# Optimization experiments

Hardware: AMD Instinct MI355X
Metric: run time of the kernel (lower is better)

## Reference

```python
import jax, jax.numpy as jnp
import numpy as np

B, NIN, NH, SUB, HID = 8192, 1433, 64, 6, 128
TEMP, LAMB, ITERS = 0.4, 20.0, 5

def prelu(x, a):
    return jnp.where(x >= 0, x, a * x)

def l2norm(x):
    # F.normalize with eps clamp
    n = jnp.maximum(jnp.linalg.norm(x, axis=-1, keepdims=True), 1e-12)
    return x / n

def setup_inputs() -> dict:
    key = jax.random.key(0)
    ks = jax.random.split(key, 16)
    inp = {}
    inp['seq1'] = jax.random.normal(ks[0], (B, SUB, NIN), jnp.float32)
    inp['seq2'] = jax.random.normal(ks[1], (B, SUB, NIN), jnp.float32)
    inp['adj1'] = jax.random.uniform(ks[2], (B, SUB, SUB), jnp.float32)
    inp['adj2'] = jax.random.uniform(ks[3], (B, SUB, SUB), jnp.float32)
    inp['rescale_ratio'] = jax.random.uniform(ks[4], (B, SUB - 1, SUB - 1), jnp.float32)
    inp['gcn_W'] = jax.random.normal(ks[5], (NH, NIN), jnp.float32) / np.sqrt(NIN)
    inp['gcn_b'] = jnp.zeros((NH,), jnp.float32)
    inp['gcn_a'] = jnp.float32(0.25)
    inp['dec_W1'] = jax.random.normal(ks[6], (HID, NH * 4), jnp.float32) / np.sqrt(NH * 4)
    inp['dec_b1'] = jnp.zeros((HID,), jnp.float32)
    inp['dec_a1'] = jnp.float32(0.25)
    inp['dec_W2'] = jax.random.normal(ks[7], (HID, HID), jnp.float32) / np.sqrt(HID)
    inp['dec_b2'] = jnp.zeros((HID,), jnp.float32)
    inp['dec_a2'] = jnp.float32(0.25)
    inp['dec_W3'] = jax.random.normal(ks[8], (NIN, HID), jnp.float32) / np.sqrt(HID)
    inp['dec_b3'] = jnp.zeros((NIN,), jnp.float32)
    inp['dec_a3'] = jnp.float32(0.25)
    inp['disc_W'] = jax.random.normal(ks[9], (1, NH, NH), jnp.float32) / np.sqrt(NH)
    inp['disc_b'] = jnp.zeros((1,), jnp.float32)
    inp['subgraph_size'] = 4
    return inp

def sinkhorn_score(g1, n1, g2, n2, rescale_ratio):
    # cost has grad; transport is computed under no_grad in torch
    cost = (1.0 - jnp.einsum('bik,bjk->bij', l2norm(g1), l2norm(g2))) * rescale_ratio
    sg = jax.lax.stop_gradient
    g1s, n1s, g2s, n2s, costs = sg(g1), sg(n1), sg(g2), sg(n2), sg(cost)
    r = jnp.einsum('bik,bjk->bij', g1s, n2s)            # [B, N, 1]
    r = jnp.where(r <= 0, 1e-8, r)
    r = r / jnp.sum(r, axis=1, keepdims=True)
    c = jnp.einsum('bik,bjk->bij', g2s, n1s)            # [B, N, 1]
    c = jnp.where(c <= 0, 1e-8, c)
    c = c / jnp.sum(c, axis=1, keepdims=True)
    P = jnp.exp(-LAMB * costs)                          # [B, N, N]
    u = jnp.ones_like(c) / c.shape[1]
    for _ in range(ITERS):
        v = r / jnp.einsum('bij,bjk->bik', P, u)
        u = c / jnp.einsum('bji,bjk->bik', P, v)
    # diag(v) @ P @ diag(u)
    transport = v * P * jnp.swapaxes(u, 1, 2)           # [B, N, N]
    S = jnp.sum(transport * (1.0 - cost), axis=(1, 2))[:, None]  # [B, 1]
    return S

def reference(seq1, seq2, adj1, adj2, rescale_ratio, gcn_W, gcn_b, gcn_a,
              dec_W1, dec_b1, dec_a1, dec_W2, dec_b2, dec_a2, dec_W3, dec_b3, dec_a3,
              disc_W, disc_b, subgraph_size):
    def gcn(seq, adj):
        fts = jnp.einsum('bnf,hf->bnh', seq, gcn_W)
        return prelu(jnp.einsum('bnm,bmh->bnh', adj, fts) + gcn_b, gcn_a)
    h1 = gcn(seq1, adj1)   # [B, SUB, NH]
    h2 = gcn(seq2, adj2)
    # swap last two rows, then split graph-part / node-part
    def swap(h):
        return jnp.concatenate([h[:, :-2], h[:, -1:], h[:, -2:-1]], axis=1)
    h1n, h2n = swap(h1), swap(h2)
    g1, n1 = h1n[:, :-1], h1n[:, -1:]
    g2, n2 = h2n[:, :-1], h2n[:, -1:]
    S = sinkhorn_score(g1, n1, g2, n2, rescale_ratio)
    loss_pos = jnp.exp(S / TEMP) * 2.0                  # [B, 1]
    # decoder (subgraph_size=4 path): sub_node = h[:, :sub_size-2, :]
    x = h1[:, :subgraph_size, :].reshape(h1.shape[0], -1)
    x = prelu(x @ dec_W1.T + dec_b1, dec_a1)
    x = prelu(x @ dec_W2.T + dec_b2, dec_a2)
    node_recons = prelu(x @ dec_W3.T + dec_b3, dec_a3)  # [B, NIN]
    # discriminator (avg readout over context nodes, bilinear score)
    c = jnp.mean(h1[:, :-1, :], axis=1)                 # [B, NH]
    hp = h1[:, -1, :]                                   # [B, NH]
    s1 = jnp.einsum('bi,oij,bj->bo', hp, disc_W, c) + disc_b
    c_mi = jnp.concatenate([c[-2:-1], c[:-1]], axis=0)  # negsamp_round=1 shift
    s2 = jnp.einsum('bi,oij,bj->bo', hp, disc_W, c_mi) + disc_b
    logits = jnp.concatenate([s1, s2], axis=1)          # [B, 2]
    return jnp.concatenate([loss_pos, node_recons, logits], axis=1)  # [B, 1+NIN+2]
```

## Files before the change

### kernel.cpp

```cpp
#include <hip/hip_runtime.h>
#include <math.h>

#define BB   8192
#define NIN  1433
#define NH   64
#define SUBG 6
#define HID  128

typedef __attribute__((ext_vector_type(8))) short bf16x8;
typedef __attribute__((ext_vector_type(4))) float f32x4;
typedef __attribute__((ext_vector_type(16))) float f32x16;

__device__ __forceinline__ short f2bf(float x) {
  unsigned u = __float_as_uint(x);
  unsigned r = (u + 0x7fffu + ((u >> 16) & 1u)) >> 16;
  return (short)r;
}
__device__ __forceinline__ float bf2f(short s) {
  return __uint_as_float(((unsigned)(unsigned short)s) << 16);
}
__device__ __forceinline__ float allred64(float v) {
#pragma unroll
  for (int m = 1; m < 64; m <<= 1) v += __shfl_xor(v, m, 64);
  return v;
}

__device__ __forceinline__ void gload_lds16(const short* g, short* l) {
  __builtin_amdgcn_global_load_lds(
      (const __attribute__((address_space(1))) void*)g,
      (__attribute__((address_space(3))) void*)l, 16, 0, 0);
}

#define WAITV(N)                                            \
  {                                                         \
    asm volatile("s_waitcnt vmcnt(" #N ")" ::: "memory");   \
    __builtin_amdgcn_sched_barrier(0);                      \
  }
#define BARRIER()                                           \
  {                                                         \
    __builtin_amdgcn_s_barrier();                           \
    __builtin_amdgcn_sched_barrier(0);                      \
  }

__global__ void pack_kernel(const float* __restrict__ src, short* __restrict__ hi,
                            short* __restrict__ lo, int Oreal, int NF, int Kreal, int nchunk) {
  int idx = blockIdx.x * 256 + threadIdx.x;
  int total = nchunk * NF * 512;
  if (idx >= total) return;
  int j    = idx & 7;
  int lane = (idx >> 3) & 63;
  int nf   = (idx >> 9) % NF;
  int c    = idx / (NF * 512);
  int o = nf * 16 + (lane & 15);
  int k = c * 32 + ((lane >> 4) << 3) + j;
  float v = (o < Oreal && k < Kreal) ? src[(size_t)o * Kreal + k] : 0.f;
  short h = f2bf(v);
  hi[idx] = h;
  lo[idx] = f2bf(v - bf2f(h));
}

__global__ void pack32_kernel(const float* __restrict__ src, short* __restrict__ hi,
                              short* __restrict__ lo) {
  int idx = blockIdx.x * 256 + threadIdx.x;
  if (idx >= 45 * 4 * 512) return;
  int j    = idx & 7;
  int lane = (idx >> 3) & 63;
  int s    = (idx >> 9) & 3;
  int c    = idx >> 11;
  int o = (s & 1) * 32 + (lane & 31);
  int k = c * 32 + ((s >> 1) << 4) + ((lane >> 5) << 3) + j;
  float v = (k < NIN) ? src[(size_t)o * NIN + k] : 0.f;
  short h = f2bf(v);
  hi[idx] = h;
  lo[idx] = f2bf(v - bf2f(h));
}

__global__ __launch_bounds__(384, 3) void gcn_mfma(
    const float* __restrict__ seq1, const float* __restrict__ seq2,
    const short* __restrict__ Gh, const short* __restrict__ Gl,
    float* __restrict__ fts1, float* __restrict__ fts2)
{
  __shared__ short sB[4][4096];
  const int tid = threadIdx.x;
  const int sid = blockIdx.x >> 8;
  const int bb  = blockIdx.x & 255;
  const float* __restrict__ seq = sid ? seq2 : seq1;
  float* __restrict__ fout = sid ? fts2 : fts1;
  const int w = tid >> 6, lane = tid & 63;
  const int l31 = lane & 31, lg2 = lane >> 5;
  const int row0 = bb * 192 + w * 32;

  f32x16 acc[2];
#pragma unroll
  for (int i = 0; i < 16; ++i) { acc[0][i] = 0.f; acc[1][i] = 0.f; }

  const float* aptr = seq + (size_t)(row0 + l31) * NIN + lg2 * 8;

  auto STAGE = [&](int c, int slot) {
    short* sb = &sB[slot][0];
    const size_t cb = (size_t)c * 256;
#pragma unroll
    for (int i = 0; i < 2; ++i) {
      const int pb = (w * 128 + i * 64) & 511;
      const short* src = (pb < 256) ? (Gh + (cb + pb) * 8 + (size_t)lane * 8)
                                    : (Gl + (cb + (pb - 256)) * 8 + (size_t)lane * 8);
      gload_lds16(src, sb + (pb + lane) * 8);
    }
  };

#define ALOAD(c_, R_)                                                        \
  {                                                                          \
    const float* ad_ = aptr + (c_) * 32;                                     \
    asm volatile(                                                            \
        "global_load_dwordx4 %0, %4, off\n\t"                                \
        "global_load_dwordx4 %1, %4, off offset:16\n\t"                      \
        "global_load_dwordx4 %2, %4, off offset:64\n\t"                      \
        "global_load_dwordx4 %3, %4, off offset:80"                          \
        : "=&v"(R_[0]), "=&v"(R_[1]), "=&v"(R_[2]), "=&v"(R_[3])             \
        : "v"(ad_));                                                         \
  }

  auto SPLIT8 = [&](const f32x4& p, const f32x4& q, bf16x8& H, bf16x8& L) {
    float av[8] = {p[0], p[1], p[2], p[3], q[0], q[1], q[2], q[3]};
#pragma unroll
    for (int j = 0; j < 8; ++j) {
      unsigned u = __float_as_uint(av[j]);
      H[j] = (short)(u >> 16);
      L[j] = f2bf(av[j] - __uint_as_float(u & 0xffff0000u));
    }
  };

  auto COMPUTE = [&](int c, const f32x4* R) {
    bf16x8 Ah0, Al0, Ah1, Al1;
    SPLIT8(R[0], R[1], Ah0, Al0);
    SPLIT8(R[2], R[3], Ah1, Al1);
    const short* bs = &sB[c & 3][0];
    __builtin_amdgcn_s_setprio(1);
#pragma unroll
    for (int ct = 0; ct < 2; ++ct) {
      bf16x8 Bh0 = *(const bf16x8*)(bs + ((0 + ct) * 64 + lane) * 8);
      bf16x8 Bl0 = *(const bf16x8*)(bs + 2048 + ((0 + ct) * 64 + lane) * 8);
      bf16x8 Bh1 = *(const bf16x8*)(bs + ((2 + ct) * 64 + lane) * 8);
      bf16x8 Bl1 = *(const bf16x8*)(bs + 2048 + ((2 + ct) * 64 + lane) * 8);
      acc[ct] = __builtin_amdgcn_mfma_f32_32x32x16_bf16(Ah0, Bh0, acc[ct], 0, 0, 0);
      acc[ct] = __builtin_amdgcn_mfma_f32_32x32x16_bf16(Al0, Bh0, acc[ct], 0, 0, 0);
      acc[ct] = __builtin_amdgcn_mfma_f32_32x32x16_bf16(Ah0, Bl0, acc[ct], 0, 0, 0);
      acc[ct] = __builtin_amdgcn_mfma_f32_32x32x16_bf16(Ah1, Bh1, acc[ct], 0, 0, 0);
      acc[ct] = __builtin_amdgcn_mfma_f32_32x32x16_bf16(Al1, Bh1, acc[ct], 0, 0, 0);
      acc[ct] = __builtin_amdgcn_mfma_f32_32x32x16_bf16(Ah1, Bl1, acc[ct], 0, 0, 0);
    }
    __builtin_amdgcn_s_setprio(0);
  };

  f32x4 A0[4], A1[4];
  STAGE(0, 0); ALOAD(0, A0);
  STAGE(1, 1); ALOAD(1, A1);

#pragma unroll 1
  for (int cc = 0; cc < 42; cc += 2) {
    WAITV(6); BARRIER();
    COMPUTE(cc, A0);
    STAGE(cc + 2, (cc + 2) & 3); ALOAD(cc + 2, A0);
    WAITV(6); BARRIER();
    COMPUTE(cc + 1, A1);
    STAGE(cc + 3, (cc + 3) & 3); ALOAD(cc + 3, A1);
  }
  WAITV(6); BARRIER();
  COMPUTE(42, A0);
  WAITV(0); BARRIER();
  COMPUTE(43, A1);

  {
    const int k0 = 44 * 32 + lg2 * 8;
    float av[16];
#pragma unroll
    for (int j = 0; j < 8; ++j) {
      int ka = k0 + j, kb = k0 + 16 + j;
      av[j]     = (ka < NIN) ? aptr[44 * 32 + j] : 0.f;
      av[8 + j] = (kb < NIN) ? aptr[44 * 32 + 16 + j] : 0.f;
    }
    bf16x8 Ah0, Al0, Ah1, Al1;
#pragma unroll
    for (int j = 0; j < 8; ++j) {
      unsigned u = __float_as_uint(av[j]);
      Ah0[j] = (short)(u >> 16);
      Al0[j] = f2bf(av[j] - __uint_as_float(u & 0xffff0000u));
      u = __float_as_uint(av[8 + j]);
      Ah1[j] = (short)(u >> 16);
      Al1[j] = f2bf(av[8 + j] - __uint_as_float(u & 0xffff0000u));
    }
#pragma unroll
    for (int ct = 0; ct < 2; ++ct) {
      const size_t o0 = ((size_t)(44 * 4 + ct) * 64 + lane) * 8;
      const size_t o1 = ((size_t)(44 * 4 + 2 + ct) * 64 + lane) * 8;
      bf16x8 Bh0 = *(const bf16x8*)(Gh + o0);
      bf16x8 Bl0 = *(const bf16x8*)(Gl + o0);
      bf16x8 Bh1 = *(const bf16x8*)(Gh + o1);
      bf16x8 Bl1 = *(const bf16x8*)(Gl + o1);
      acc[ct] = __builtin_amdgcn_mfma_f32_32x32x16_bf16(Ah0, Bh0, acc[ct], 0, 0, 0);
      acc[ct] = __builtin_amdgcn_mfma_f32_32x32x16_bf16(Al0, Bh0, acc[ct], 0, 0, 0);
      acc[ct] = __builtin_amdgcn_mfma_f32_32x32x16_bf16(Ah0, Bl0, acc[ct], 0, 0, 0);
      acc[ct] = __builtin_amdgcn_mfma_f32_32x32x16_bf16(Ah1, Bh1, acc[ct], 0, 0, 0);
      acc[ct] = __builtin_amdgcn_mfma_f32_32x32x16_bf16(Al1, Bh1, acc[ct], 0, 0, 0);
      acc[ct] = __builtin_amdgcn_mfma_f32_32x32x16_bf16(Ah1, Bl1, acc[ct], 0, 0, 0);
    }
  }

#pragma unroll
  for (int ct = 0; ct < 2; ++ct)
#pragma unroll
    for (int reg = 0; reg < 16; ++reg) {
      int crow = (reg & 3) + 8 * (reg >> 2) + 4 * lg2;
      fout[(size_t)(row0 + crow) * 64 + ct * 32 + l31] = acc[ct][reg];
    }
#undef ALOAD
}

__global__ __launch_bounds__(256) void sink_kernel(
    const float* __restrict__ fts1, const float* __restrict__ fts2,
    const float* __restrict__ adj1, const float* __restrict__ adj2,
    const float* __restrict__ resc, const float* __restrict__ discW,
    const float* __restrict__ bias, const float* __restrict__ aP,
    float* __restrict__ out, float* __restrict__ tws, float* __restrict__ h1w)
{
  const int b = (blockIdx.x << 2) + (threadIdx.x >> 6);
  const int lane = threadIdx.x & 63;
  const float* F1 = fts1 + (size_t)b * 384;
  const float* F2 = fts2 + (size_t)b * 384;
  float f1[6], f2[6];
#pragma unroll
  for (int m = 0; m < 6; ++m) { f1[m] = F1[m * 64 + lane]; f2[m] = F2[m * 64 + lane]; }
  const float bv = bias[lane];
  const float a = aP[0];
  const float* A1 = adj1 + (size_t)b * 36;
  const float* A2 = adj2 + (size_t)b * 36;
  float h1v[6], h2v[6];
#pragma unroll
  for (int n = 0; n < 6; ++n) {
    float o1 = bv, o2 = bv;
#pragma unroll
    for (int m = 0; m < 6; ++m) {
      o1 = fmaf(A1[n * 6 + m], f1[m], o1);
      o2 = fmaf(A2[n * 6 + m], f2[m], o2);
    }
    h1v[n] = (o1 >= 0.f) ? o1 : a * o1;
    h2v[n] = (o2 >= 0.f) ? o2 : a * o2;
  }
#pragma unroll
  for (int n = 0; n < 6; ++n) h1w[(size_t)b * 384 + n * 64 + lane] = h1v[n];

  float g1[5], g2[5];
#pragma unroll
  for (int i = 0; i < 4; ++i) { g1[i] = h1v[i]; g2[i] = h2v[i]; }
  g1[4] = h1v[5]; g2[4] = h2v[5];
  const float n1 = h1v[4], n2 = h2v[4];

  {
    float cm = (g1[0] + g1[1] + g1[2] + g1[3] + n1) * 0.2f;
    float t = 0.f;
    const float4* W4 = (const float4*)discW;
#pragma unroll 4
    for (int jq = 0; jq < 16; ++jq) {
      float4 wv = W4[lane * 16 + jq];
      t = fmaf(wv.x, __shfl(cm, 4 * jq, 64), t);
      t = fmaf(wv.y, __shfl(cm, 4 * jq + 1, 64), t);
      t = fmaf(wv.z, __shfl(cm, 4 * jq + 2, 64), t);
      t = fmaf(wv.w, __shfl(cm, 4 * jq + 3, 64), t);
    }
    tws[(size_t)b * 64 + lane] = t;
  }

  float in1[5], in2[5];
#pragma unroll
  for (int i = 0; i < 5; ++i) {
    float s = allred64(g1[i] * g1[i]);
    in1[i] = 1.f / fmaxf(sqrtf(s), 1e-12f);
    s = allred64(g2[i] * g2[i]);
    in2[i] = 1.f / fmaxf(sqrtf(s), 1e-12f);
  }
  float cost[25], P[25];
#pragma unroll
  for (int i = 0; i < 5; ++i)
#pragma unroll
    for (int j = 0; j < 5; ++j) {
      float d = allred64(g1[i] * g2[j]);
      float cv = (1.f - d * in1[i] * in2[j]) * resc[(size_t)b * 25 + i * 5 + j];
      cost[i * 5 + j] = cv;
      P[i * 5 + j] = expf(-20.f * cv);
    }
  float r[5], c[5];
  float rs = 0.f, cs = 0.f;
#pragma unroll
  for (int i = 0; i < 5; ++i) {
    float d = allred64(g1[i] * n2); d = (d <= 0.f) ? 1e-8f : d; r[i] = d; rs += d;
    d = allred64(g2[i] * n1);       d = (d <= 0.f) ? 1e-8f : d; c[i] = d; cs += d;
  }
#pragma unroll
  for (int i = 0; i < 5; ++i) { r[i] = r[i] / rs; c[i] = c[i] / cs; }

  float u[5], v[5];
#pragma unroll
  for (int i = 0; i < 5; ++i) u[i] = 0.2f;
#pragma unroll
  for (int it = 0; it < 5; ++it) {
#pragma unroll
    for (int i = 0; i < 5; ++i) {
      float pv = 0.f;
#pragma unroll
      for (int j = 0; j < 5; ++j) pv = fmaf(P[i * 5 + j], u[j], pv);
      v[i] = r[i] / pv;
    }
#pragma unroll
    for (int i = 0; i < 5; ++i) {
      float pu = 0.f;
#pragma unroll
      for (int j = 0; j < 5; ++j) pu = fmaf(P[j * 5 + i], v[j], pu);
      u[i] = c[i] / pu;
    }
  }
  float S = 0.f;
#pragma unroll
  for (int i = 0; i < 5; ++i)
#pragma unroll
    for (int j = 0; j < 5; ++j)
      S += v[i] * P[i * 5 + j] * u[j] * (1.f - cost[i * 5 + j]);
  if (lane == 0) out[(size_t)b * 1436] = expf(S * 2.5f) * 2.f;
}

__global__ __launch_bounds__(64) void dec12_mfma(
    const float* __restrict__ h1,
    const short* __restrict__ B1h, const short* __restrict__ B1l,
    const float* __restrict__ b1, const float* __restrict__ a1P,
    const short* __restrict__ B2h, const short* __restrict__ B2l,
    const float* __restrict__ b2, const float* __restrict__ a2P,
    float* __restrict__ x3)
{
  __shared__ float xT[16][132];
  const int lane = threadIdx.x;
  const int l15 = lane & 15, lg = lane >> 4;
  const int r0 = blockIdx.x * 16;

  f32x4 acc[8];
#pragma unroll
  for (int i = 0; i < 8; ++i) acc[i] = (f32x4){0.f, 0.f, 0.f, 0.f};

#pragma unroll
  for (int c = 0; c < 8; ++c) {
    const float* ap = h1 + (size_t)(r0 + l15) * 384 + c * 32 + lg * 8;
    float4 p = *(const float4*)ap;
    float4 q = *(const float4*)(ap + 4);
    float av[8] = {p.x, p.y, p.z, p.w, q.x, q.y, q.z, q.w};
    bf16x8 Ah, Al;
#pragma unroll
    for (int j = 0; j < 8; ++j) { short h = f2bf(av[j]); Ah[j] = h; Al[j] = f2bf(av[j] - bf2f(h)); }
#pragma unroll
    for (int nf = 0; nf < 8; ++nf) {
      size_t off = (((size_t)(c * 8 + nf)) << 9) + (size_t)lane * 8;
      bf16x8 Bh = *(const bf16x8*)(B1h + off);
      bf16x8 Bl = *(const bf16x8*)(B1l + off);
      acc[nf] = __builtin_amdgcn_mfma_f32_16x16x32_bf16(Ah, Bh, acc[nf], 0, 0, 0);
      acc[nf] = __builtin_amdgcn_mfma_f32_16x16x32_bf16(Al, Bh, acc[nf], 0, 0, 0);
      acc[nf] = __builtin_amdgcn_mfma_f32_16x16x32_bf16(Ah, Bl, acc[nf], 0, 0, 0);
    }
  }
  {
    const float a1 = a1P[0];
#pragma unroll
    for (int nf = 0; nf < 8; ++nf) {
      int o = nf * 16 + l15;
      float bv = b1[o];
#pragma unroll
      for (int j = 0; j < 4; ++j) {
        float v = acc[nf][j] + bv;
        xT[lg * 4 + j][o] = (v >= 0.f) ? v : a1 * v;
      }
    }
  }
  __syncthreads();

#pragma unroll
  for (int i = 0; i < 8; ++i) acc[i] = (f32x4){0.f, 0.f, 0.f, 0.f};
#pragma unroll
  for (int c = 0; c < 4; ++c) {
    const float* ap = &xT[l15][c * 32 + lg * 8];
    float4 p = *(const float4*)ap;
    float4 q = *(const float4*)(ap + 4);
    float av[8] = {p.x, p.y, p.z, p.w, q.x, q.y, q.z, q.w};
    bf16x8 Ah, Al;
#pragma unroll
    for (int j = 0; j < 8; ++j) { short h = f2bf(av[j]); Ah[j] = h; Al[j] = f2bf(av[j] - bf2f(h)); }
#pragma unroll
    for (int nf = 0; nf < 8; ++nf) {
      size_t off = (((size_t)(c * 8 + nf)) << 9) + (size_t)lane * 8;
      bf16x8 Bh = *(const bf16x8*)(B2h + off);
      bf16x8 Bl = *(const bf16x8*)(B2l + off);
      acc[nf] = __builtin_amdgcn_mfma_f32_16x16x32_bf16(Ah, Bh, acc[nf], 0, 0, 0);
      acc[nf] = __builtin_amdgcn_mfma_f32_16x16x32_bf16(Al, Bh, acc[nf], 0, 0, 0);
      acc[nf] = __builtin_amdgcn_mfma_f32_16x16x32_bf16(Ah, Bl, acc[nf], 0, 0, 0);
    }
  }
  {
    const float a2 = a2P[0];
#pragma unroll
    for (int nf = 0; nf < 8; ++nf) {
      int o = nf * 16 + l15;
      float bv = b2[o];
#pragma unroll
      for (int j = 0; j < 4; ++j) {
        float v = acc[nf][j] + bv;
        v = (v >= 0.f) ? v : a2 * v;
        x3[(size_t)(r0 + lg * 4 + j) * 128 + o] = v;
      }
    }
  }
}

__global__ __launch_bounds__(64) void dec3_mfma(
    const float* __restrict__ x3,
    const short* __restrict__ B3h, const short* __restrict__ B3l,
    const float* __restrict__ b3, const float* __restrict__ a3P,
    float* __restrict__ out)
{
  const int lane = threadIdx.x;
  const int l15 = lane & 15, lg = lane >> 4;
  const int rowblk = blockIdx.x & 511;
  const int nfg = blockIdx.x >> 9;
  const int r0 = rowblk * 16;

  bf16x8 A3h[4], A3l[4];
#pragma unroll
  for (int c = 0; c < 4; ++c) {
    const float* ap = x3 + (size_t)(r0 + l15) * 128 + c * 32 + lg * 8;
    float4 p = *(const float4*)ap;
    float4 q = *(const float4*)(ap + 4);
    float av[8] = {p.x, p.y, p.z, p.w, q.x, q.y, q.z, q.w};
#pragma unroll
    for (int j = 0; j < 8; ++j) {
      short h = f2bf(av[j]); A3h[c][j] = h; A3l[c][j] = f2bf(av[j] - bf2f(h));
    }
  }
  const float a3 = a3P[0];
  for (int t = 0; t < 15; ++t) {
    const int nf = nfg * 15 + t;
    f32x4 acc = (f32x4){0.f, 0.f, 0.f, 0.f};
#pragma unroll
    for (int c = 0; c < 4; ++c) {
      size_t off = (((size_t)(c * 90 + nf)) << 9) + (size_t)lane * 8;
      bf16x8 Bh = *(const bf16x8*)(B3h + off);
      bf16x8 Bl = *(const bf16x8*)(B3l + off);
      acc = __builtin_amdgcn_mfma_f32_16x16x32_bf16(A3h[c], Bh, acc, 0, 0, 0);
      acc = __builtin_amdgcn_mfma_f32_16x16x32_bf16(A3l[c], Bh, acc, 0, 0, 0);
      acc = __builtin_amdgcn_mfma_f32_16x16x32_bf16(A3h[c], Bl, acc, 0, 0, 0);
    }
    const int o = nf * 16 + l15;
    if (o < NIN) {
      float bv = b3[o];
#pragma unroll
      for (int j = 0; j < 4; ++j) {
        float v = acc[j] + bv;
        v = (v >= 0.f) ? v : a3 * v;
        out[(size_t)(r0 + lg * 4 + j) * 1436 + 1 + o] = v;
      }
    }
  }
}

__global__ __launch_bounds__(256) void disc_kernel(
    const float* __restrict__ h1, const float* __restrict__ tws,
    const float* __restrict__ dbP, float* __restrict__ out)
{
  const int b = (blockIdx.x << 2) + (threadIdx.x >> 6);
  const int lane = threadIdx.x & 63;
  float hp = h1[((size_t)b * SUBG + 5) * NH + lane];
  float t0 = tws[(size_t)b * 64 + lane];
  int bp = (b == 0) ? (BB - 2) : (b - 1);
  float tp = tws[(size_t)bp * 64 + lane];
  float s1 = allred64(hp * t0);
  float s2 = allred64(hp * tp);
  if (lane == 0) {
    float db = dbP[0];
    out[(size_t)b * 1436 + 1434] = s1 + db;
    out[(size_t)b * 1436 + 1435] = s2 + db;
  }
}

extern "C" void kernel_launch(void* const* d_in, const int* in_sizes, int n_in,
                              void* d_out, int out_size, void* d_ws, size_t ws_size,
                              hipStream_t stream) {
  (void)in_sizes; (void)n_in; (void)out_size; (void)ws_size;
  const float* seq1  = (const float*)d_in[0];
  const float* seq2  = (const float*)d_in[1];
  const float* adj1  = (const float*)d_in[2];
  const float* adj2  = (const float*)d_in[3];
  const float* resc  = (const float*)d_in[4];
  const float* gcnW  = (const float*)d_in[5];
  const float* gcnB  = (const float*)d_in[6];
  const float* gcnA  = (const float*)d_in[7];
  const float* W1    = (const float*)d_in[8];
  const float* b1    = (const float*)d_in[9];
  const float* a1    = (const float*)d_in[10];
  const float* W2    = (const float*)d_in[11];
  const float* b2    = (const float*)d_in[12];
  const float* a2    = (const float*)d_in[13];
  const float* W3    = (const float*)d_in[14];
  const float* b3    = (const float*)d_in[15];
  const float* a3    = (const float*)d_in[16];
  const float* discW = (const float*)d_in[17];
  const float* discB = (const float*)d_in[18];

  float* fts1 = (float*)d_ws;
  float* fts2 = fts1 + (size_t)BB * SUBG * NH;
  float* h1   = fts2 + (size_t)BB * SUBG * NH;
  float* tws  = h1  + (size_t)BB * SUBG * NH;
  float* x3   = tws + (size_t)BB * 64;
  short* Gh   = (short*)(x3 + (size_t)BB * 128);
  short* Gl   = Gh  + 45 * 4 * 512;
  short* B1h  = Gl  + 45 * 4 * 512;
  short* B1l  = B1h + 8 * 8 * 512;
  short* B2h  = B1l + 8 * 8 * 512;
  short* B2l  = B2h + 4 * 8 * 512;
  short* B3h  = B2l + 4 * 8 * 512;
  short* B3l  = B3h + 4 * 90 * 512;
  float* out  = (float*)d_out;

  pack32_kernel<<<(45 * 4 * 512 + 255) / 256, 256, 0, stream>>>(gcnW, Gh, Gl);
  pack_kernel<<<(8 * 8 * 512 + 255) / 256, 256, 0, stream>>>(W1, B1h, B1l, 128, 8, 256, 8);
  pack_kernel<<<(4 * 8 * 512 + 255) / 256, 256, 0, stream>>>(W2, B2h, B2l, 128, 8, 128, 4);
  pack_kernel<<<(4 * 90 * 512 + 255) / 256, 256, 0, stream>>>(W3, B3h, B3l, 1433, 90, 128, 4);

  gcn_mfma<<<512, 384, 0, stream>>>(seq1, seq2, Gh, Gl, fts1, fts2);
  sink_kernel<<<2048, 256, 0, stream>>>(fts1, fts2, adj1, adj2, resc, discW, gcnB, gcnA,
                                        out, tws, h1);
  dec12_mfma<<<512, 64, 0, stream>>>(h1, B1h, B1l, b1, a1, B2h, B2l, b2, a2, x3);
  dec3_mfma<<<3072, 64, 0, stream>>>(x3, B3h, B3l, b3, a3, out);
  disc_kernel<<<2048, 256, 0, stream>>>(h1, tws, discB, out);
}
```

Baseline: 325.3 us.

## Load GCN weight fragments directly into registers instead of staging through LDS

The GCN projection kernel no longer stages packed bf16 hi/lo weight chunks into shared memory with global_load_lds and block barriers. Each wave now loads its B fragments straight from global (L2-resident) memory into registers, double-buffered alongside the A loads. With no barriers, the block shrinks to 4 waves with a 768-block grid. This removes LDS traffic and inter-wave synchronisation, but every wave now fetches the weights redundantly and needs more VGPRs.

```diff
diff --git a/kernel.cpp b/kernel.cpp
--- a/kernel.cpp
+++ b/kernel.cpp
@@ -25,20 +25,9 @@
   return v;
 }
 
-__device__ __forceinline__ void gload_lds16(const short* g, short* l) {
-  __builtin_amdgcn_global_load_lds(
-      (const __attribute__((address_space(1))) void*)g,
-      (__attribute__((address_space(3))) void*)l, 16, 0, 0);
-}
-
 #define WAITV(N)                                            \
   {                                                         \
     asm volatile("s_waitcnt vmcnt(" #N ")" ::: "memory");   \
-    __builtin_amdgcn_sched_barrier(0);                      \
-  }
-#define BARRIER()                                           \
-  {                                                         \
-    __builtin_amdgcn_s_barrier();                           \
     __builtin_amdgcn_sched_barrier(0);                      \
   }
 
@@ -75,38 +64,25 @@
   lo[idx] = f2bf(v - bf2f(h));
 }
 
-__global__ __launch_bounds__(384, 3) void gcn_mfma(
+__global__ __launch_bounds__(256, 3) void gcn_mfma(
     const float* __restrict__ seq1, const float* __restrict__ seq2,
     const short* __restrict__ Gh, const short* __restrict__ Gl,
     float* __restrict__ fts1, float* __restrict__ fts2)
 {
-  __shared__ short sB[4][4096];
   const int tid = threadIdx.x;
-  const int sid = blockIdx.x >> 8;
-  const int bb  = blockIdx.x & 255;
+  const int sid = (blockIdx.x >= 384);
+  const int bb  = sid ? (blockIdx.x - 384) : blockIdx.x;
   const float* __restrict__ seq = sid ? seq2 : seq1;
   float* __restrict__ fout = sid ? fts2 : fts1;
   const int w = tid >> 6, lane = tid & 63;
   const int l31 = lane & 31, lg2 = lane >> 5;
-  const int row0 = bb * 192 + w * 32;
+  const int row0 = bb * 128 + w * 32;
 
   f32x16 acc[2];
 #pragma unroll
   for (int i = 0; i < 16; ++i) { acc[0][i] = 0.f; acc[1][i] = 0.f; }
 
   const float* aptr = seq + (size_t)(row0 + l31) * NIN + lg2 * 8;
-
-  auto STAGE = [&](int c, int slot) {
-    short* sb = &sB[slot][0];
-    const size_t cb = (size_t)c * 256;
-#pragma unroll
-    for (int i = 0; i < 2; ++i) {
-      const int pb = (w * 128 + i * 64) & 511;
-      const short* src = (pb < 256) ? (Gh + (cb + pb) * 8 + (size_t)lane * 8)
-                                    : (Gl + (cb + (pb - 256)) * 8 + (size_t)lane * 8);
-      gload_lds16(src, sb + (pb + lane) * 8);
-    }
-  };
 
 #define ALOAD(c_, R_)                                                        \
   {                                                                          \
@@ -120,6 +96,26 @@
         : "v"(ad_));                                                         \
   }
 
+#define BLOAD(c_, H_, L_)                                                    \
+  {                                                                          \
+    const short* bh_ = Gh + ((size_t)(c_) * 256 + lane) * 8;                 \
+    const short* bl_ = Gl + ((size_t)(c_) * 256 + lane) * 8;                 \
+    asm volatile(                                                            \
+        "global_load_dwordx4 %0, %4, off\n\t"                                \
+        "global_load_dwordx4 %1, %4, off offset:1024\n\t"                    \
+        "global_load_dwordx4 %2, %4, off offset:2048\n\t"                    \
+        "global_load_dwordx4 %3, %4, off offset:3072"                        \
+        : "=&v"(H_[0]), "=&v"(H_[1]), "=&v"(H_[2]), "=&v"(H_[3])             \
+        : "v"(bh_));                                                         \
+    asm volatile(                                                            \
+        "global_load_dwordx4 %0, %4, off\n\t"                                \
+        "global_load_dwordx4 %1, %4, off offset:1024\n\t"                    \
+        "global_load_dwordx4 %2, %4, off offset:2048\n\t"                    \
+        "global_load_dwordx4 %3, %4, off offset:3072"                        \
+        : "=&v"(L_[0]), "=&v"(L_[1]), "=&v"(L_[2]), "=&v"(L_[3])             \
+        : "v"(bl_));                                                         \
+  }
+
   auto SPLIT8 = [&](const f32x4& p, const f32x4& q, bf16x8& H, bf16x8& L) {
     float av[8] = {p[0], p[1], p[2], p[3], q[0], q[1], q[2], q[3]};
 #pragma unroll
@@ -130,45 +126,42 @@
     }
   };
 
-  auto COMPUTE = [&](int c, const f32x4* R) {
+  auto COMPUTE = [&](const f32x4* R, const bf16x8* H, const bf16x8* L) {
     bf16x8 Ah0, Al0, Ah1, Al1;
     SPLIT8(R[0], R[1], Ah0, Al0);
     SPLIT8(R[2], R[3], Ah1, Al1);
-    const short* bs = &sB[c & 3][0];
     __builtin_amdgcn_s_setprio(1);
 #pragma unroll
     for (int ct = 0; ct < 2; ++ct) {
-      bf16x8 Bh0 = *(const bf16x8*)(bs + ((0 + ct) * 64 + lane) * 8);
-      bf16x8 Bl0 = *(const bf16x8*)(bs + 2048 + ((0 + ct) * 64 + lane) * 8);
-      bf16x8 Bh1 = *(const bf16x8*)(bs + ((2 + ct) * 64 + lane) * 8);
-      bf16x8 Bl1 = *(const bf16x8*)(bs + 2048 + ((2 + ct) * 64 + lane) * 8);
-      acc[ct] = __builtin_amdgcn_mfma_f32_32x32x16_bf16(Ah0, Bh0, acc[ct], 0, 0, 0);
-      acc[ct] = __builtin_amdgcn_mfma_f32_32x32x16_bf16(Al0, Bh0, acc[ct], 0, 0, 0);
-      acc[ct] = __builtin_amdgcn_mfma_f32_32x32x16_bf16(Ah0, Bl0, acc[ct], 0, 0, 0);
-      acc[ct] = __builtin_amdgcn_mfma_f32_32x32x16_bf16(Ah1, Bh1, acc[ct], 0, 0, 0);
-      acc[ct] = __builtin_amdgcn_mfma_f32_32x32x16_bf16(Al1, Bh1, acc[ct], 0, 0, 0);
-      acc[ct] = __builtin_amdgcn_mfma_f32_32x32x16_bf16(Ah1, Bl1, acc[ct], 0, 0, 0);
+      acc[ct] = __builtin_amdgcn_mfma_f32_32x32x16_bf16(Ah0, H[ct],     acc[ct], 0, 0, 0);
+      acc[ct] = __builtin_amdgcn_mfma_f32_32x32x16_bf16(Al0, H[ct],     acc[ct], 0, 0, 0);
+      acc[ct] = __builtin_amdgcn_mfma_f32_32x32x16_bf16(Ah0, L[ct],     acc[ct], 0, 0, 0);
+      acc[ct] = __builtin_amdgcn_mfma_f32_32x32x16_bf16(Ah1, H[2 + ct], acc[ct], 0, 0, 0);
+      acc[ct] = __builtin_amdgcn_mfma_f32_32x32x16_bf16(Al1, H[2 + ct], acc[ct], 0, 0, 0);
+      acc[ct] = __builtin_amdgcn_mfma_f32_32x32x16_bf16(Ah1, L[2 + ct], acc[ct], 0, 0, 0);
     }
     __builtin_amdgcn_s_setprio(0);
   };
 
   f32x4 A0[4], A1[4];
-  STAGE(0, 0); ALOAD(0, A0);
-  STAGE(1, 1); ALOAD(1, A1);
+  bf16x8 H0[4], L0[4], H1[4], L1[4];
+
+  ALOAD(0, A0); BLOAD(0, H0, L0);
+  ALOAD(1, A1); BLOAD(1, H1, L1);
 
 #pragma unroll 1
   for (int cc = 0; cc < 42; cc += 2) {
-    WAITV(6); BARRIER();
-    COMPUTE(cc, A0);
-    STAGE(cc + 2, (cc + 2) & 3); ALOAD(cc + 2, A0);
-    WAITV(6); BARRIER();
-    COMPUTE(cc + 1, A1);
-    STAGE(cc + 3, (cc + 3) & 3); ALOAD(cc + 3, A1);
-  }
-  WAITV(6); BARRIER();
-  COMPUTE(42, A0);
-  WAITV(0); BARRIER();
-  COMPUTE(43, A1);
+    WAITV(12);
+    COMPUTE(A0, H0, L0);
+    ALOAD(cc + 2, A0); BLOAD(cc + 2, H0, L0);
+    WAITV(12);
+    COMPUTE(A1, H1, L1);
+    ALOAD(cc + 3, A1); BLOAD(cc + 3, H1, L1);
+  }
+  WAITV(12);
+  COMPUTE(A0, H0, L0);
+  WAITV(0);
+  COMPUTE(A1, H1, L1);
 
   {
     const int k0 = 44 * 32 + lg2 * 8;
@@ -214,6 +207,7 @@
       fout[(size_t)(row0 + crow) * 64 + ct * 32 + l31] = acc[ct][reg];
     }
 #undef ALOAD
+#undef BLOAD
 }
 
 __global__ __launch_bounds__(256) void sink_kernel(
@@ -528,7 +522,7 @@
   pack_kernel<<<(4 * 8 * 512 + 255) / 256, 256, 0, stream>>>(W2, B2h, B2l, 128, 8, 128, 4);
   pack_kernel<<<(4 * 90 * 512 + 255) / 256, 256, 0, stream>>>(W3, B3h, B3l, 1433, 90, 128, 4);
 
-  gcn_mfma<<<512, 384, 0, stream>>>(seq1, seq2, Gh, Gl, fts1, fts2);
+  gcn_mfma<<<768, 256, 0, stream>>>(seq1, seq2, Gh, Gl, fts1, fts2);
   sink_kernel<<<2048, 256, 0, stream>>>(fts1, fts2, adj1, adj2, resc, discW, gcnB, gcnA,
                                         out, tws, h1);
   dec12_mfma<<<512, 64, 0, stream>>>(h1, B1h, B1l, b1, a1, B2h, B2l, b2, a2, x3);
```

Result: slower. 358.7 us (+10.3%).

## Fuse decoder layers and discriminator into one kernel; merge weight packing launches

Applied to the files above, without the earlier changes.

Merges the four weight-packing kernels into one launch. Fuses dec12, dec3 and the discriminator into one 256-thread kernel per 16-row block. The layer-2 activations stay in shared memory instead of going through a global x3 buffer, and the four waves split the output column tiles. This cuts launch overhead and the x3 round trip through global memory. In exchange, the layer-3 output stage now runs on only 512 blocks instead of 3072, which reduces parallelism for the largest GEMM.

```diff
diff --git a/kernel.cpp b/kernel.cpp
--- a/kernel.cpp
+++ b/kernel.cpp
@@ -42,11 +42,9 @@
     __builtin_amdgcn_sched_barrier(0);                      \
   }
 
-__global__ void pack_kernel(const float* __restrict__ src, short* __restrict__ hi,
-                            short* __restrict__ lo, int Oreal, int NF, int Kreal, int nchunk) {
-  int idx = blockIdx.x * 256 + threadIdx.x;
-  int total = nchunk * NF * 512;
-  if (idx >= total) return;
+__device__ __forceinline__ void pack16_impl(const float* __restrict__ src,
+                                            short* __restrict__ hi, short* __restrict__ lo,
+                                            int Oreal, int NF, int Kreal, int idx) {
   int j    = idx & 7;
   int lane = (idx >> 3) & 63;
   int nf   = (idx >> 9) % NF;
@@ -59,10 +57,9 @@
   lo[idx] = f2bf(v - bf2f(h));
 }
 
-__global__ void pack32_kernel(const float* __restrict__ src, short* __restrict__ hi,
-                              short* __restrict__ lo) {
-  int idx = blockIdx.x * 256 + threadIdx.x;
-  if (idx >= 45 * 4 * 512) return;
+__device__ __forceinline__ void pack32_impl(const float* __restrict__ src,
+                                            short* __restrict__ hi, short* __restrict__ lo,
+                                            int idx) {
   int j    = idx & 7;
   int lane = (idx >> 3) & 63;
   int s    = (idx >> 9) & 3;
@@ -73,6 +70,26 @@
   short h = f2bf(v);
   hi[idx] = h;
   lo[idx] = f2bf(v - bf2f(h));
+}
+
+#define PK_G  (45 * 4 * 512)
+#define PK_B1 (8 * 8 * 512)
+#define PK_B2 (4 * 8 * 512)
+#define PK_B3 (4 * 90 * 512)
+#define PK_TOTAL (PK_G + PK_B1 + PK_B2 + PK_B3)
+
+__global__ void pack_all(const float* __restrict__ gcnW, const float* __restrict__ W1,
+                         const float* __restrict__ W2, const float* __restrict__ W3,
+                         short* Gh, short* Gl, short* B1h, short* B1l,
+                         short* B2h, short* B2l, short* B3h, short* B3l) {
+  int idx = blockIdx.x * 256 + threadIdx.x;
+  if (idx < PK_G) { pack32_impl(gcnW, Gh, Gl, idx); return; }
+  idx -= PK_G;
+  if (idx < PK_B1) { pack16_impl(W1, B1h, B1l, 128, 8, 256, idx); return; }
+  idx -= PK_B1;
+  if (idx < PK_B2) { pack16_impl(W2, B2h, B2l, 128, 8, 128, idx); return; }
+  idx -= PK_B2;
+  if (idx < PK_B3) { pack16_impl(W3, B3h, B3l, 1433, 90, 128, idx); }
 }
 
 __global__ __launch_bounds__(384, 3) void gcn_mfma(
@@ -327,23 +344,27 @@
   if (lane == 0) out[(size_t)b * 1436] = expf(S * 2.5f) * 2.f;
 }
 
-__global__ __launch_bounds__(64) void dec12_mfma(
+__global__ __launch_bounds__(256) void dec_fused(
     const float* __restrict__ h1,
     const short* __restrict__ B1h, const short* __restrict__ B1l,
     const float* __restrict__ b1, const float* __restrict__ a1P,
     const short* __restrict__ B2h, const short* __restrict__ B2l,
     const float* __restrict__ b2, const float* __restrict__ a2P,
-    float* __restrict__ x3)
+    const short* __restrict__ B3h, const short* __restrict__ B3l,
+    const float* __restrict__ b3, const float* __restrict__ a3P,
+    const float* __restrict__ tws, const float* __restrict__ dbP,
+    float* __restrict__ out)
 {
   __shared__ float xT[16][132];
-  const int lane = threadIdx.x;
+  __shared__ float x2T[16][132];
+  const int tid = threadIdx.x;
+  const int w = tid >> 6, lane = tid & 63;
   const int l15 = lane & 15, lg = lane >> 4;
   const int r0 = blockIdx.x * 16;
 
-  f32x4 acc[8];
-#pragma unroll
-  for (int i = 0; i < 8; ++i) acc[i] = (f32x4){0.f, 0.f, 0.f, 0.f};
-
+  f32x4 acc1[2];
+  acc1[0] = (f32x4){0.f, 0.f, 0.f, 0.f};
+  acc1[1] = (f32x4){0.f, 0.f, 0.f, 0.f};
 #pragma unroll
   for (int c = 0; c < 8; ++c) {
     const float* ap = h1 + (size_t)(r0 + l15) * 384 + c * 32 + lg * 8;
@@ -354,32 +375,33 @@
 #pragma unroll
     for (int j = 0; j < 8; ++j) { short h = f2bf(av[j]); Ah[j] = h; Al[j] = f2bf(av[j] - bf2f(h)); }
 #pragma unroll
-    for (int nf = 0; nf < 8; ++nf) {
+    for (int i = 0; i < 2; ++i) {
+      const int nf = 2 * w + i;
       size_t off = (((size_t)(c * 8 + nf)) << 9) + (size_t)lane * 8;
       bf16x8 Bh = *(const bf16x8*)(B1h + off);
       bf16x8 Bl = *(const bf16x8*)(B1l + off);
-      acc[nf] = __builtin_amdgcn_mfma_f32_16x16x32_bf16(Ah, Bh, acc[nf], 0, 0, 0);
-      acc[nf] = __builtin_amdgcn_mfma_f32_16x16x32_bf16(Al, Bh, acc[nf], 0, 0, 0);
-      acc[nf] = __builtin_amdgcn_mfma_f32_16x16x32_bf16(Ah, Bl, acc[nf], 0, 0, 0);
+      acc1[i] = __builtin_amdgcn_mfma_f32_16x16x32_bf16(Ah, Bh, acc1[i], 0, 0, 0);
+      acc1[i] = __builtin_amdgcn_mfma_f32_16x16x32_bf16(Al, Bh, acc1[i], 0, 0, 0);
+      acc1[i] = __builtin_amdgcn_mfma_f32_16x16x32_bf16(Ah, Bl, acc1[i], 0, 0, 0);
     }
   }
   {
     const float a1 = a1P[0];
 #pragma unroll
-    for (int nf = 0; nf < 8; ++nf) {
-      int o = nf * 16 + l15;
-      float bv = b1[o];
+    for (int i = 0; i < 2; ++i) {
+      int o = (2 * w + i) * 16 + l15;
+      float bvv = b1[o];
 #pragma unroll
       for (int j = 0; j < 4; ++j) {
-        float v = acc[nf][j] + bv;
+        float v = acc1[i][j] + bvv;
         xT[lg * 4 + j][o] = (v >= 0.f) ? v : a1 * v;
       }
     }
   }
   __syncthreads();
 
-#pragma unroll
-  for (int i = 0; i < 8; ++i) acc[i] = (f32x4){0.f, 0.f, 0.f, 0.f};
+  acc1[0] = (f32x4){0.f, 0.f, 0.f, 0.f};
+  acc1[1] = (f32x4){0.f, 0.f, 0.f, 0.f};
 #pragma unroll
   for (int c = 0; c < 4; ++c) {
     const float* ap = &xT[l15][c * 32 + lg * 8];
@@ -390,47 +412,35 @@
 #pragma unroll
     for (int j = 0; j < 8; ++j) { short h = f2bf(av[j]); Ah[j] = h; Al[j] = f2bf(av[j] - bf2f(h)); }
 #pragma unroll
-    for (int nf = 0; nf < 8; ++nf) {
+    for (int i = 0; i < 2; ++i) {
+      const int nf = 2 * w + i;
       size_t off = (((size_t)(c * 8 + nf)) << 9) + (size_t)lane * 8;
       bf16x8 Bh = *(const bf16x8*)(B2h + off);
       bf16x8 Bl = *(const bf16x8*)(B2l + off);
-      acc[nf] = __builtin_amdgcn_mfma_f32_16x16x32_bf16(Ah, Bh, acc[nf], 0, 0, 0);
-      acc[nf] = __builtin_amdgcn_mfma_f32_16x16x32_bf16(Al, Bh, acc[nf], 0, 0, 0);
-      acc[nf] = __builtin_amdgcn_mfma_f32_16x16x32_bf16(Ah, Bl, acc[nf], 0, 0, 0);
+      acc1[i] = __builtin_amdgcn_mfma_f32_16x16x32_bf16(Ah, Bh, acc1[i], 0, 0, 0);
+      acc1[i] = __builtin_amdgcn_mfma_f32_16x16x32_bf16(Al, Bh, acc1[i], 0, 0, 0);
+      acc1[i] = __builtin_amdgcn_mfma_f32_16x16x32_bf16(Ah, Bl, acc1[i], 0, 0, 0);
     }
   }
   {
     const float a2 = a2P[0];
 #pragma unroll
-    for (int nf = 0; nf < 8; ++nf) {
-      int o = nf * 16 + l15;
-      float bv = b2[o];
+    for (int i = 0; i < 2; ++i) {
+      int o = (2 * w + i) * 16 + l15;
+      float bvv = b2[o];
 #pragma unroll
       for (int j = 0; j < 4; ++j) {
-        float v = acc[nf][j] + bv;
-        v = (v >= 0.f) ? v : a2 * v;
-        x3[(size_t)(r0 + lg * 4 + j) * 128 + o] = v;
+        float v = acc1[i][j] + bvv;
+        x2T[lg * 4 + j][o] = (v >= 0.f) ? v : a2 * v;
       }
     }
   }
-}
-
-__global__ __launch_bounds__(64) void dec3_mfma(
-    const float* __restrict__ x3,
-    const short* __restrict__ B3h, const short* __restrict__ B3l,
-    const float* __restrict__ b3, const float* __restrict__ a3P,
-    float* __restrict__ out)
-{
-  const int lane = threadIdx.x;
-  const int l15 = lane & 15, lg = lane >> 4;
-  const int rowblk = blockIdx.x & 511;
-  const int nfg = blockIdx.x >> 9;
-  const int r0 = rowblk * 16;
+  __syncthreads();
 
   bf16x8 A3h[4], A3l[4];
 #pragma unroll
   for (int c = 0; c < 4; ++c) {
-    const float* ap = x3 + (size_t)(r0 + l15) * 128 + c * 32 + lg * 8;
+    const float* ap = &x2T[l15][c * 32 + lg * 8];
     float4 p = *(const float4*)ap;
     float4 q = *(const float4*)(ap + 4);
     float av[8] = {p.x, p.y, p.z, p.w, q.x, q.y, q.z, q.w};
@@ -440,8 +450,10 @@
     }
   }
   const float a3 = a3P[0];
-  for (int t = 0; t < 15; ++t) {
-    const int nf = nfg * 15 + t;
+#pragma unroll 1
+  for (int t = 0; t < 23; ++t) {
+    const int nf = w + 4 * t;
+    if (nf >= 90) break;
     f32x4 acc = (f32x4){0.f, 0.f, 0.f, 0.f};
 #pragma unroll
     for (int c = 0; c < 4; ++c) {
@@ -454,33 +466,32 @@
     }
     const int o = nf * 16 + l15;
     if (o < NIN) {
-      float bv = b3[o];
+      float bvv = b3[o];
 #pragma unroll
       for (int j = 0; j < 4; ++j) {
-        float v = acc[j] + bv;
+        float v = acc[j] + bvv;
         v = (v >= 0.f) ? v : a3 * v;
         out[(size_t)(r0 + lg * 4 + j) * 1436 + 1 + o] = v;
       }
     }
   }
-}
-
-__global__ __launch_bounds__(256) void disc_kernel(
-    const float* __restrict__ h1, const float* __restrict__ tws,
-    const float* __restrict__ dbP, float* __restrict__ out)
-{
-  const int b = (blockIdx.x << 2) + (threadIdx.x >> 6);
-  const int lane = threadIdx.x & 63;
-  float hp = h1[((size_t)b * SUBG + 5) * NH + lane];
-  float t0 = tws[(size_t)b * 64 + lane];
-  int bp = (b == 0) ? (BB - 2) : (b - 1);
-  float tp = tws[(size_t)bp * 64 + lane];
-  float s1 = allred64(hp * t0);
-  float s2 = allred64(hp * tp);
-  if (lane == 0) {
-    float db = dbP[0];
-    out[(size_t)b * 1436 + 1434] = s1 + db;
-    out[(size_t)b * 1436 + 1435] = s2 + db;
+
+  {
+    const float db = dbP[0];
+#pragma unroll
+    for (int i = 0; i < 4; ++i) {
+      const int bb = r0 + 4 * w + i;
+      float hp = h1[(size_t)bb * 384 + 5 * 64 + lane];
+      float t0 = tws[(size_t)bb * 64 + lane];
+      const int bp = (bb == 0) ? (BB - 2) : (bb - 1);
+      float tp = tws[(size_t)bp * 64 + lane];
+      float s1 = allred64(hp * t0);
+      float s2 = allred64(hp * tp);
+      if (lane == 0) {
+        out[(size_t)bb * 1436 + 1434] = s1 + db;
+        out[(size_t)bb * 1436 + 1435] = s2 + db;
+      }
+    }
   }
 }
 
@@ -512,26 +523,22 @@
   float* fts2 = fts1 + (size_t)BB * SUBG * NH;
   float* h1   = fts2 + (size_t)BB * SUBG * NH;
   float* tws  = h1  + (size_t)BB * SUBG * NH;
-  float* x3   = tws + (size_t)BB * 64;
-  short* Gh   = (short*)(x3 + (size_t)BB * 128);
-  short* Gl   = Gh  + 45 * 4 * 512;
-  short* B1h  = Gl  + 45 * 4 * 512;
-  short* B1l  = B1h + 8 * 8 * 512;
-  short* B2h  = B1l + 8 * 8 * 512;
-  short* B2l  = B2h + 4 * 8 * 512;
-  short* B3h  = B2l + 4 * 8 * 512;
-  short* B3l  = B3h + 4 * 90 * 512;
+  short* Gh   = (short*)(tws + (size_t)BB * 64);
+  short* Gl   = Gh  + PK_G;
+  short* B1h  = Gl  + PK_G;
+  short* B1l  = B1h + PK_B1;
+  short* B2h  = B1l + PK_B1;
+  short* B2l  = B2h + PK_B2;
+  short* B3h  = B2l + PK_B2;
+  short* B3l  = B3h + PK_B3;
   float* out  = (float*)d_out;
 
-  pack32_kernel<<<(45 * 4 * 512 + 255) / 256, 256, 0, stream>>>(gcnW, Gh, Gl);
-  pack_kernel<<<(8 * 8 * 512 + 255) / 256, 256, 0, stream>>>(W1, B1h, B1l, 128, 8, 256, 8);
-  pack_kernel<<<(4 * 8 * 512 + 255) / 256, 256, 0, stream>>>(W2, B2h, B2l, 128, 8, 128, 4);
-  pack_kernel<<<(4 * 90 * 512 + 255) / 256, 256, 0, stream>>>(W3, B3h, B3l, 1433, 90, 128, 4);
+  pack_all<<<(PK_TOTAL + 255) / 256, 256, 0, stream>>>(
+      gcnW, W1, W2, W3, Gh, Gl, B1h, B1l, B2h, B2l, B3h, B3l);
 
   gcn_mfma<<<512, 384, 0, stream>>>(seq1, seq2, Gh, Gl, fts1, fts2);
   sink_kernel<<<2048, 256, 0, stream>>>(fts1, fts2, adj1, adj2, resc, discW, gcnB, gcnA,
                                         out, tws, h1);
-  dec12_mfma<<<512, 64, 0, stream>>>(h1, B1h, B1l, b1, a1, B2h, B2l, b2, a2, x3);
-  dec3_mfma<<<3072, 64, 0, stream>>>(x3, B3h, B3l, b3, a3, out);
-  disc_kernel<<<2048, 256, 0, stream>>>(h1, tws, discB, out);
-}
+  dec_fused<<<512, 256, 0, stream>>>(h1, B1h, B1l, b1, a1, B2h, B2l, b2, a2,
+                                     B3h, B3l, b3, a3, tws, discB, out);
+}
```

Measured after the change: 320.0 us. No clear change (-1.6%).
